# Kernel tuning notes

Hardware: AMD Instinct MI355X
Metric: run time of the kernel (lower is better)

## Reference

```python
import jax, jax.numpy as jnp
import numpy as np

# FlowNetC correlation hyperparameters (match init_kwargs)
PAD = 20          # pad_size
KSIZE = 1         # kernel_size (1x1 patches -> plain per-pixel dot over channels)
MAXD = 20         # max_displacement
STRIDE1 = 1       # output grid stride
STRIDE2 = 2       # displacement stride


def setup_inputs() -> dict:
    key = jax.random.key(0)
    k1, k2 = jax.random.split(key)
    B, C, H, W = 16, 256, 48, 64
    return {
        "input1": jax.random.normal(k1, (B, C, H, W), dtype=jnp.float32),
        "input2": jax.random.normal(k2, (B, C, H, W), dtype=jnp.float32),
    }


def _correlation(in1, in2):
    B, C, H, W = in1.shape
    # pad input2 spatially; max_displacement == pad_size so every shifted
    # window of size (H, W) stays in-bounds of the padded map.
    pad2 = jnp.pad(in2, ((0, 0), (0, 0), (PAD, PAD), (PAD, PAD)))
    disps = np.arange(-MAXD, MAXD + 1, STRIDE2)  # 21 offsets per axis
    offsets = jnp.asarray(
        [(PAD + dy, PAD + dx) for dy in disps for dx in disps], dtype=jnp.int32
    )  # [D=441, 2]

    in1s = in1[:, :, ::STRIDE1, ::STRIDE1]  # output-grid view of input1

    def one_displacement(off):
        # shifted (H, W) window of padded input2 at displacement (dy, dx)
        sl = jax.lax.dynamic_slice(pad2, (0, 0, off[0], off[1]), (B, C, H, W))
        sl = sl[:, :, ::STRIDE1, ::STRIDE1]
        # per-pixel dot product over channels
        return jnp.einsum('bchw,bchw->bhw', in1s, sl)

    # lax.map keeps memory low: one [B,C,H,W] slice live at a time
    out = jax.lax.map(one_displacement, offsets)  # [D, B, Ho, Wo]
    sumelems = KSIZE * KSIZE * C  # CUDA kernel normalizes by patch elem count
    return jnp.transpose(out, (1, 0, 2, 3)) / sumelems  # [B, D, Ho, Wo]


def reference(input1, input2):
    return _correlation(input1, input2)
```

## Files before the change

### kernel.cpp

```cpp
#include <hip/hip_runtime.h>
#include <stdint.h>

#define NB 16
#define NC 256
#define NH 48
#define NW 64
#define ND 21
#define HW (NH * NW)
#define ROW_ELEMS (NW * NC)
#define SOUT_LD (NW + 1)
#define SOUT_SZ (ND * SOUT_LD)
#define NXCD 8
#define NWG (NB * NH)

typedef __bf16 bf16x8 __attribute__((ext_vector_type(8)));
typedef float f32x4 __attribute__((ext_vector_type(4)));

__device__ __forceinline__ int xcd_wg(int orig) {
    return (orig & (NXCD - 1)) * (NWG / NXCD) + (orig >> 3);
}

__device__ __forceinline__ int sw_addr(int x, int chunk) {
    int cs = (chunk & ~7) | ((chunk ^ x) & 7);
    return x * 256 + (cs << 3);
}
__device__ __forceinline__ int posx(int x) { return ((x & 1) << 5) | (x >> 1); }

__device__ __forceinline__ int frag_off(int w, int kb, int l) {
    return w * 4096 + kb * 512 + ((l ^ ((w & 3) << 1)) << 3);
}

__device__ __forceinline__ bf16x8 load_pack8(const float* __restrict__ p, int cbase) {
    bf16x8 v;
#pragma unroll
    for (int j = 0; j < 8; ++j)
        v[j] = (__bf16)p[(size_t)(cbase + j) * HW];
    return v;
}

__global__ void __launch_bounds__(256, 4)
convert_in2(const float* __restrict__ in2, unsigned short* __restrict__ ws) {
    __shared__ unsigned short s[ROW_ELEMS];
    const int tid = threadIdx.x;
    const int wg = xcd_wg(blockIdx.x);
    const int b = wg / NH, y = wg % NH;
    const int x = tid & 63, g0 = tid >> 6;
    const int par = x & 1, m_lo = (x >> 1) & 15, nt = x >> 5;
    const int w = (nt << 1) | par;
    const float* p = in2 + ((size_t)b * NC * NH + y) * NW + x;
#pragma unroll
    for (int i = 0; i < 8; ++i) {
        const int chunk = g0 * 8 + i;
        const int kb = chunk >> 2, quad = chunk & 3;
        const int l = (quad << 4) | m_lo;
        bf16x8 v = load_pack8(p, chunk * 8);
        *(bf16x8*)&s[frag_off(w, kb, l)] = v;
    }
    __syncthreads();
    unsigned short* wr = ws + ((size_t)b * NH + y) * ROW_ELEMS;
#pragma unroll
    for (int i = 0; i < 8; ++i) {
        const int e = (i * 256 + tid) * 8;
        *(bf16x8*)(wr + e) = *(const bf16x8*)(s + e);
    }
}

__global__ void __launch_bounds__(256, 3)
corr_main(const float* __restrict__ in1, const unsigned short* __restrict__ ws,
          float* __restrict__ out) {
    __shared__ unsigned short s1[ROW_ELEMS];
    __shared__ float sout[2 * SOUT_SZ];
    const int tid  = threadIdx.x;
    const int wg   = xcd_wg(blockIdx.x);
    const int b    = wg / NH, y = wg % NH;
    const int lane = tid & 63, wave = tid >> 6;
    const int m_lo = lane & 15, quad = lane >> 4;
    const int par  = wave & 1, nt = wave >> 1;

    {
        const int x = tid & 63, g0 = tid >> 6;
        const int px = posx(x);
        const float* p = in1 + ((size_t)b * NC * NH + y) * NW + x;
#pragma unroll
        for (int i = 0; i < 8; ++i) {
            const int chunk = g0 * 8 + i;
            bf16x8 v = load_pack8(p, chunk * 8);
            *(bf16x8*)&s1[sw_addr(px, chunk)] = v;
        }
    }
    for (int i = tid; i < 2 * SOUT_SZ; i += 256) sout[i] = 0.0f;

    const int d0 = (y >= 20) ? 0 : (21 - y) >> 1;
    const int d1 = min(20, (67 - y) >> 1);
    const unsigned short* wsb = ws + (size_t)b * NH * ROW_ELEMS;
    const int slice_off = frag_off(wave, 0, lane);

    auto load_b = [&](bf16x8 (&bf)[8], int dyi) {
        const unsigned short* row = wsb + (size_t)(y - 20 + 2 * dyi) * ROW_ELEMS + slice_off;
#pragma unroll
        for (int kb = 0; kb < 8; ++kb)
            bf[kb] = *(const bf16x8*)&row[kb * 512];
    };

    bf16x8 bfA[8], bfB[8];
    load_b(bfA, d0);
    __syncthreads();

    bf16x8 afrag[2][8];
#pragma unroll
    for (int mm = 0; mm < 2; ++mm) {
        const int pos = par * 32 + 16 * mm + m_lo;
#pragma unroll
        for (int kb = 0; kb < 8; ++kb)
            afrag[mm][kb] = *(const bf16x8*)&s1[sw_addr(pos, 4 * kb + quad)];
    }

    float* outbase = out + (((size_t)b * (ND * ND)) * NH + (size_t)y) * NW;
    for (int dyi = 0; dyi < ND; ++dyi) {
        if (dyi >= d0 && dyi <= d1) continue;
        float* ob = outbase + (size_t)dyi * ND * HW;
        for (int i = tid; i < ND * NW; i += 256)
            __builtin_nontemporal_store(0.0f, &ob[(size_t)(i >> 6) * HW + (i & 63)]);
    }

    const float scale = 1.0f / 256.0f;
    const int xq  = 4 * quad;
    const int xph = 16 * nt + m_lo;
    const int dx0 = tid & 63;
    const int dp0 = tid >> 6;

    auto step = [&](bf16x8 (&bc)[8], bf16x8 (&bn)[8], int dyi, int cb) {
        if (dyi < d1) load_b(bn, dyi + 1);

        const bool have = dyi > d0;
        float dv[6];
        float* sp = sout + (cb ^ 1) * SOUT_SZ;
        if (have) {
#pragma unroll
            for (int k = 0; k < 6; ++k) {
                const int i = dx0 + (dp0 + 4 * k) * 64;
                if (i < ND * NW) dv[k] = sp[(dp0 + 4 * k) * SOUT_LD + dx0];
            }
        }

        f32x4 acc0 = {0.f, 0.f, 0.f, 0.f}, acc1 = {0.f, 0.f, 0.f, 0.f};
#pragma unroll
        for (int kb = 0; kb < 8; ++kb) {
            acc0 = __builtin_amdgcn_mfma_f32_16x16x32_bf16(afrag[0][kb], bc[kb], acc0, 0, 0, 0);
            acc1 = __builtin_amdgcn_mfma_f32_16x16x32_bf16(afrag[1][kb], bc[kb], acc1, 0, 0, 0);
        }

        if (have) {
            float* ob = outbase + (size_t)(dyi - 1) * ND * HW;
#pragma unroll
            for (int k = 0; k < 6; ++k) {
                const int i = dx0 + (dp0 + 4 * k) * 64;
                if (i < ND * NW)
                    __builtin_nontemporal_store(dv[k] * scale,
                                                &ob[(size_t)(dp0 + 4 * k) * HW + dx0]);
            }
        }

        float* sb = sout + cb * SOUT_SZ;
#pragma unroll
        for (int r = 0; r < 4; ++r) {
            {
                const int xh = xq + r;
                const int dxi = xph - xh + 10;
                if ((unsigned)dxi <= 20u) sb[dxi * SOUT_LD + 2 * xh + par] = acc0[r];
            }
            {
                const int xh = 16 + xq + r;
                const int dxi = xph - xh + 10;
                if ((unsigned)dxi <= 20u) sb[dxi * SOUT_LD + 2 * xh + par] = acc1[r];
            }
        }
        __asm__ __volatile__("s_waitcnt lgkmcnt(0)\n\ts_barrier" ::: "memory");
    };

    int dyi = d0, last;
    while (true) {
        step(bfA, bfB, dyi, 0);
        if (++dyi > d1) { last = 0; break; }
        step(bfB, bfA, dyi, 1);
        if (++dyi > d1) { last = 1; break; }
    }
    {
        float* sp = sout + last * SOUT_SZ;
        float* ob = outbase + (size_t)d1 * ND * HW;
        for (int i = tid; i < ND * NW; i += 256) {
            const int pl = i >> 6, x = i & 63;
            __builtin_nontemporal_store(sp[pl * SOUT_LD + x] * scale, &ob[(size_t)pl * HW + x]);
        }
    }
}

__global__ void __launch_bounds__(256, 2)
corr_fallback(const float* __restrict__ in1, const float* __restrict__ in2,
              float* __restrict__ out) {
    __shared__ unsigned short s1[ROW_ELEMS];
    __shared__ unsigned short s2[ROW_ELEMS];
    const int tid = threadIdx.x;
    const int b = blockIdx.x / NH, y = blockIdx.x % NH;
    const int lane = tid & 63, wave = tid >> 6;
    const int m_lo = lane & 15, quad = lane >> 4;
    const int asub = wave >> 1, bsub = wave & 1;
    {
        const int x = tid & 63, g0 = tid >> 6;
        const float* p = in1 + ((size_t)b * NC * NH + y) * NW + x;
        for (int i = 0; i < 8; ++i) {
            const int chunk = g0 * 8 + i;
            bf16x8 v = load_pack8(p, chunk * 8);
            *(bf16x8*)&s1[sw_addr(x, chunk)] = v;
        }
    }
    __syncthreads();
    bf16x8 afrag[2][8];
    for (int mm = 0; mm < 2; ++mm) {
        const int x = 32 * asub + 16 * mm + m_lo;
        for (int kb = 0; kb < 8; ++kb)
            afrag[mm][kb] = *(const bf16x8*)&s1[sw_addr(x, 4 * kb + quad)];
    }
    const float scale = 1.0f / 256.0f;
    for (int dyi = 0; dyi < ND; ++dyi) {
        const int ys = y + 2 * dyi - 20;
        float* ob = out + (((size_t)b * (ND * ND) + (size_t)dyi * ND) * NH + y) * NW;
        if ((unsigned)ys >= (unsigned)NH) {
            for (int i = tid; i < ND * NW; i += 256)
                ob[(size_t)(i >> 6) * HW + (i & 63)] = 0.0f;
            continue;
        }
        __syncthreads();
        {
            const int x = tid & 63, g0 = tid >> 6;
            const float* p = in2 + ((size_t)b * NC * NH + ys) * NW + x;
            for (int i = 0; i < 8; ++i) {
                const int chunk = g0 * 8 + i;
                bf16x8 v = load_pack8(p, chunk * 8);
                *(bf16x8*)&s2[sw_addr(x, chunk)] = v;
            }
        }
        __syncthreads();
        f32x4 acc[2][2];
        for (int mm = 0; mm < 2; ++mm)
            for (int nn = 0; nn < 2; ++nn) acc[mm][nn] = (f32x4){0.f, 0.f, 0.f, 0.f};
        for (int nn = 0; nn < 2; ++nn) {
            const int xpp = 32 * bsub + 16 * nn + m_lo;
            for (int kb = 0; kb < 8; ++kb) {
                bf16x8 bfrag = *(const bf16x8*)&s2[sw_addr(xpp, 4 * kb + quad)];
                acc[0][nn] = __builtin_amdgcn_mfma_f32_16x16x32_bf16(afrag[0][kb], bfrag, acc[0][nn], 0, 0, 0);
                acc[1][nn] = __builtin_amdgcn_mfma_f32_16x16x32_bf16(afrag[1][kb], bfrag, acc[1][nn], 0, 0, 0);
            }
        }
        for (int mm = 0; mm < 2; ++mm)
            for (int nn = 0; nn < 2; ++nn) {
                const int xb = 32 * asub + 16 * mm + 4 * quad;
                const int xpp = 32 * bsub + 16 * nn + m_lo;
                for (int r = 0; r < 4; ++r) {
                    const int x = xb + r, d = xpp - x;
                    if (d >= -20 && d <= 20 && !(d & 1))
                        ob[(size_t)((d + 20) >> 1) * HW + x] = acc[mm][nn][r] * scale;
                }
            }
        for (int i = tid; i < ND * 20; i += 256) {
            const int dxi = i / 20, j = i - dxi * 20;
            const int dx = 2 * dxi - 20, a = dx < 0 ? -dx : dx;
            if (j < a) {
                const int x = dx < 0 ? j : (NW - dx + j);
                ob[(size_t)dxi * HW + x] = 0.0f;
            }
        }
    }
}

extern "C" void kernel_launch(void* const* d_in, const int* in_sizes, int n_in,
                              void* d_out, int out_size, void* d_ws, size_t ws_size,
                              hipStream_t stream) {
    const float* in1 = (const float*)d_in[0];
    const float* in2 = (const float*)d_in[1];
    float* out = (float*)d_out;
    const size_t need = (size_t)NB * NH * ROW_ELEMS * sizeof(unsigned short);
    if (ws_size >= need) {
        convert_in2<<<dim3(NWG), dim3(256), 0, stream>>>(in2, (unsigned short*)d_ws);
        corr_main<<<dim3(NWG), dim3(256), 0, stream>>>(in1, (const unsigned short*)d_ws, out);
    } else {
        corr_fallback<<<dim3(NWG), dim3(256), 0, stream>>>(in1, in2, out);
    }
}
```

Measured before the change: 55.74 us.

## Process two vertical displacements per barrier phase in correlation kernel

Restructures the main loop so each phase computes two dy displacements at once, with three rotating B-fragment register buffers and a 4-slot shared output buffer, halving the number of barriers and store phases. A-fragments are now reloaded from LDS inside the MFMA loop instead of being held in registers, to free registers for the extra buffers. Output padding (SOUT_LD) is dropped, which may add LDS bank conflicts, and LDS use doubles, which could lower occupancy.

Result: slower. 69.61 us (+24.9%).

```diff
diff --git a/kernel.cpp b/kernel.cpp
--- a/kernel.cpp
+++ b/kernel.cpp
@@ -8,8 +8,6 @@
 #define ND 21
 #define HW (NH * NW)
 #define ROW_ELEMS (NW * NC)
-#define SOUT_LD (NW + 1)
-#define SOUT_SZ (ND * SOUT_LD)
 #define NXCD 8
 #define NWG (NB * NH)
 
@@ -69,7 +67,7 @@
 corr_main(const float* __restrict__ in1, const unsigned short* __restrict__ ws,
           float* __restrict__ out) {
     __shared__ unsigned short s1[ROW_ELEMS];
-    __shared__ float sout[2 * SOUT_SZ];
+    __shared__ float sout[4][ND * NW];
     const int tid  = threadIdx.x;
     const int wg   = xcd_wg(blockIdx.x);
     const int b    = wg / NH, y = wg % NH;
@@ -88,7 +86,7 @@
             *(bf16x8*)&s1[sw_addr(px, chunk)] = v;
         }
     }
-    for (int i = tid; i < 2 * SOUT_SZ; i += 256) sout[i] = 0.0f;
+    for (int i = tid; i < 4 * ND * NW; i += 256) ((float*)sout)[i] = 0.0f;
 
     const int d0 = (y >= 20) ? 0 : (21 - y) >> 1;
     const int d1 = min(20, (67 - y) >> 1);
@@ -102,18 +100,10 @@
             bf[kb] = *(const bf16x8*)&row[kb * 512];
     };
 
-    bf16x8 bfA[8], bfB[8];
-    load_b(bfA, d0);
+    bf16x8 B0[8], B1[8], B2[8];
+    load_b(B0, d0);
+    load_b(B1, d0 + 1);
     __syncthreads();
-
-    bf16x8 afrag[2][8];
-#pragma unroll
-    for (int mm = 0; mm < 2; ++mm) {
-        const int pos = par * 32 + 16 * mm + m_lo;
-#pragma unroll
-        for (int kb = 0; kb < 8; ++kb)
-            afrag[mm][kb] = *(const bf16x8*)&s1[sw_addr(pos, 4 * kb + quad)];
-    }
 
     float* outbase = out + (((size_t)b * (ND * ND)) * NH + (size_t)y) * NW;
     for (int dyi = 0; dyi < ND; ++dyi) {
@@ -124,73 +114,103 @@
     }
 
     const float scale = 1.0f / 256.0f;
-    const int xq  = 4 * quad;
-    const int xph = 16 * nt + m_lo;
-    const int dx0 = tid & 63;
-    const int dp0 = tid >> 6;
-
-    auto step = [&](bf16x8 (&bc)[8], bf16x8 (&bn)[8], int dyi, int cb) {
-        if (dyi < d1) load_b(bn, dyi + 1);
-
-        const bool have = dyi > d0;
-        float dv[6];
-        float* sp = sout + (cb ^ 1) * SOUT_SZ;
+    const int xq    = 4 * quad;
+    const int xph   = 16 * nt + m_lo;
+    const int apos0 = par * 32 + m_lo;
+    const int apos1 = par * 32 + 16 + m_lo;
+
+    auto phase = [&](bf16x8 (&bc0)[8], bf16x8 (&bc1)[8], bf16x8 (&bn)[8],
+                     int p, bool have, int cb) {
+        const bool two = (p + 1 <= d1);
+
+        float dva[6], dvb[6];
         if (have) {
-#pragma unroll
-            for (int k = 0; k < 6; ++k) {
-                const int i = dx0 + (dp0 + 4 * k) * 64;
-                if (i < ND * NW) dv[k] = sp[(dp0 + 4 * k) * SOUT_LD + dx0];
-            }
-        }
-
-        f32x4 acc0 = {0.f, 0.f, 0.f, 0.f}, acc1 = {0.f, 0.f, 0.f, 0.f};
+            const float* spa = sout[2 * (cb ^ 1)];
+            const float* spb = sout[2 * (cb ^ 1) + 1];
+#pragma unroll
+            for (int k = 0; k < 5; ++k) {
+                dva[k] = spa[(wave + 4 * k) * NW + lane];
+                dvb[k] = spb[(wave + 4 * k) * NW + lane];
+            }
+            if (wave == 0) { dva[5] = spa[20 * NW + lane]; dvb[5] = spb[20 * NW + lane]; }
+        }
+
+        f32x4 a00 = {0,0,0,0}, a01 = {0,0,0,0}, a10 = {0,0,0,0}, a11 = {0,0,0,0};
 #pragma unroll
         for (int kb = 0; kb < 8; ++kb) {
-            acc0 = __builtin_amdgcn_mfma_f32_16x16x32_bf16(afrag[0][kb], bc[kb], acc0, 0, 0, 0);
-            acc1 = __builtin_amdgcn_mfma_f32_16x16x32_bf16(afrag[1][kb], bc[kb], acc1, 0, 0, 0);
-        }
+            bf16x8 af0 = *(const bf16x8*)&s1[sw_addr(apos0, 4 * kb + quad)];
+            bf16x8 af1 = *(const bf16x8*)&s1[sw_addr(apos1, 4 * kb + quad)];
+            a00 = __builtin_amdgcn_mfma_f32_16x16x32_bf16(af0, bc0[kb], a00, 0, 0, 0);
+            a01 = __builtin_amdgcn_mfma_f32_16x16x32_bf16(af1, bc0[kb], a01, 0, 0, 0);
+            a10 = __builtin_amdgcn_mfma_f32_16x16x32_bf16(af0, bc1[kb], a10, 0, 0, 0);
+            a11 = __builtin_amdgcn_mfma_f32_16x16x32_bf16(af1, bc1[kb], a11, 0, 0, 0);
+        }
+
+        if (p + 2 <= d1) load_b(bn, p + 2);
+        if (p + 3 <= d1) load_b(bc1, p + 3);
 
         if (have) {
-            float* ob = outbase + (size_t)(dyi - 1) * ND * HW;
-#pragma unroll
-            for (int k = 0; k < 6; ++k) {
-                const int i = dx0 + (dp0 + 4 * k) * 64;
-                if (i < ND * NW)
-                    __builtin_nontemporal_store(dv[k] * scale,
-                                                &ob[(size_t)(dp0 + 4 * k) * HW + dx0]);
-            }
-        }
-
-        float* sb = sout + cb * SOUT_SZ;
+            float* oba = outbase + (size_t)(p - 2) * ND * HW;
+            float* obb = outbase + (size_t)(p - 1) * ND * HW;
+#pragma unroll
+            for (int k = 0; k < 5; ++k) {
+                __builtin_nontemporal_store(dva[k] * scale, &oba[(size_t)(wave + 4 * k) * HW + lane]);
+                __builtin_nontemporal_store(dvb[k] * scale, &obb[(size_t)(wave + 4 * k) * HW + lane]);
+            }
+            if (wave == 0) {
+                __builtin_nontemporal_store(dva[5] * scale, &oba[(size_t)20 * HW + lane]);
+                __builtin_nontemporal_store(dvb[5] * scale, &obb[(size_t)20 * HW + lane]);
+            }
+        }
+
+        float* sb0 = sout[2 * cb];
+        float* sb1 = sout[2 * cb + 1];
 #pragma unroll
         for (int r = 0; r < 4; ++r) {
             {
                 const int xh = xq + r;
                 const int dxi = xph - xh + 10;
-                if ((unsigned)dxi <= 20u) sb[dxi * SOUT_LD + 2 * xh + par] = acc0[r];
+                if ((unsigned)dxi <= 20u) {
+                    const int a = dxi * NW + 2 * xh + par;
+                    sb0[a] = a00[r];
+                    if (two) sb1[a] = a10[r];
+                }
             }
             {
                 const int xh = 16 + xq + r;
                 const int dxi = xph - xh + 10;
-                if ((unsigned)dxi <= 20u) sb[dxi * SOUT_LD + 2 * xh + par] = acc1[r];
+                if ((unsigned)dxi <= 20u) {
+                    const int a = dxi * NW + 2 * xh + par;
+                    sb0[a] = a01[r];
+                    if (two) sb1[a] = a11[r];
+                }
             }
         }
         __asm__ __volatile__("s_waitcnt lgkmcnt(0)\n\ts_barrier" ::: "memory");
     };
 
-    int dyi = d0, last;
+    int p = d0;
+    bool have = false;
+    int lastcb, lastp;
     while (true) {
-        step(bfA, bfB, dyi, 0);
-        if (++dyi > d1) { last = 0; break; }
-        step(bfB, bfA, dyi, 1);
-        if (++dyi > d1) { last = 1; break; }
+        phase(B0, B1, B2, p, have, 0);
+        have = true; lastp = p; p += 2;
+        if (p > d1) { lastcb = 0; break; }
+        phase(B2, B1, B0, p, true, 1);
+        lastp = p; p += 2;
+        if (p > d1) { lastcb = 1; break; }
     }
     {
-        float* sp = sout + last * SOUT_SZ;
-        float* ob = outbase + (size_t)d1 * ND * HW;
+        const bool two = (lastp + 1 <= d1);
+        const float* spa = sout[2 * lastcb];
+        const float* spb = sout[2 * lastcb + 1];
+        float* oba = outbase + (size_t)lastp * ND * HW;
+        float* obb = outbase + (size_t)(lastp + 1) * ND * HW;
         for (int i = tid; i < ND * NW; i += 256) {
             const int pl = i >> 6, x = i & 63;
-            __builtin_nontemporal_store(sp[pl * SOUT_LD + x] * scale, &ob[(size_t)pl * HW + x]);
+            __builtin_nontemporal_store(spa[pl * NW + x] * scale, &oba[(size_t)pl * HW + x]);
+            if (two)
+                __builtin_nontemporal_store(spb[pl * NW + x] * scale, &obb[(size_t)pl * HW + x]);
         }
     }
 }
```

## Split correlation workgroups by x-half and dy-half for more parallelism

Applied to the files above, without the earlier changes.

Each (batch,row) workgroup of corr_main is split into four: two halves of the x range (mt) and two halves of the dy displacement range. Each block now holds half of input1's row in LDS and runs one MFMA accumulator per step instead of two. It reuses the same shared buffer for the input fragment and the output staging, which cuts LDS use and raises the occupancy target to 4. In exchange, the B-fragment rows are loaded redundantly by the x-half blocks, and extra barriers plus four times as many launches add overhead.

Result: slower. 58.96 us (+5.8%).

```diff
diff --git a/kernel.cpp b/kernel.cpp
--- a/kernel.cpp
+++ b/kernel.cpp
@@ -8,23 +8,27 @@
 #define ND 21
 #define HW (NH * NW)
 #define ROW_ELEMS (NW * NC)
-#define SOUT_LD (NW + 1)
-#define SOUT_SZ (ND * SOUT_LD)
 #define NXCD 8
 #define NWG (NB * NH)
+#define SO_LD 33
+#define SO_SZ (ND * SO_LD)
 
 typedef __bf16 bf16x8 __attribute__((ext_vector_type(8)));
 typedef float f32x4 __attribute__((ext_vector_type(4)));
 
 __device__ __forceinline__ int xcd_wg(int orig) {
     return (orig & (NXCD - 1)) * (NWG / NXCD) + (orig >> 3);
+}
+
+__device__ __forceinline__ int swh(int lpos, int chunk) {
+    int cs = (chunk & ~7) | ((chunk ^ lpos) & 7);
+    return lpos * 256 + (cs << 3);
 }
 
 __device__ __forceinline__ int sw_addr(int x, int chunk) {
     int cs = (chunk & ~7) | ((chunk ^ x) & 7);
     return x * 256 + (cs << 3);
 }
-__device__ __forceinline__ int posx(int x) { return ((x & 1) << 5) | (x >> 1); }
 
 __device__ __forceinline__ int frag_off(int w, int kb, int l) {
     return w * 4096 + kb * 512 + ((l ^ ((w & 3) << 1)) << 3);
@@ -65,36 +69,59 @@
     }
 }
 
-__global__ void __launch_bounds__(256, 3)
+__global__ void __launch_bounds__(256, 4)
 corr_main(const float* __restrict__ in1, const unsigned short* __restrict__ ws,
           float* __restrict__ out) {
-    __shared__ unsigned short s1[ROW_ELEMS];
-    __shared__ float sout[2 * SOUT_SZ];
+    __shared__ __align__(16) unsigned char smem[16384];
+    unsigned short* s1h = (unsigned short*)smem;
+    float* soutf = (float*)smem;
+
     const int tid  = threadIdx.x;
-    const int wg   = xcd_wg(blockIdx.x);
+    const int xcd  = blockIdx.x & 7;
+    const int u    = blockIdx.x >> 3;
+    const int wg   = xcd * (NWG / NXCD) + (u >> 2);
+    const int mt   = u & 1, half = (u >> 1) & 1;
     const int b    = wg / NH, y = wg % NH;
     const int lane = tid & 63, wave = tid >> 6;
     const int m_lo = lane & 15, quad = lane >> 4;
     const int par  = wave & 1, nt = wave >> 1;
 
-    {
-        const int x = tid & 63, g0 = tid >> 6;
-        const int px = posx(x);
-        const float* p = in1 + ((size_t)b * NC * NH + y) * NW + x;
-#pragma unroll
-        for (int i = 0; i < 8; ++i) {
-            const int chunk = g0 * 8 + i;
-            bf16x8 v = load_pack8(p, chunk * 8);
-            *(bf16x8*)&s1[sw_addr(px, chunk)] = v;
-        }
-    }
-    for (int i = tid; i < 2 * SOUT_SZ; i += 256) sout[i] = 0.0f;
-
     const int d0 = (y >= 20) ? 0 : (21 - y) >> 1;
     const int d1 = min(20, (67 - y) >> 1);
+    const int r0 = half * 11, r1 = half ? ND : 11;
+    const int e0 = max(d0, r0), e1 = min(d1, r1 - 1);
+
+    float* outbase = out + (((size_t)b * (ND * ND)) * NH + (size_t)y) * NW;
+    const int xl = tid & 31, dpz = tid >> 5;
+
+    auto zero_plane = [&](int dyi) {
+        float* ob = outbase + (size_t)dyi * ND * HW;
+#pragma unroll
+        for (int k = 0; k < 3; ++k) {
+            const int dxi = dpz + 8 * k;
+            if (dxi < ND)
+                __builtin_nontemporal_store(0.0f, &ob[(size_t)dxi * HW + 32 * mt + xl]);
+        }
+    };
+    if (e0 > e1) {
+        for (int dyi = r0; dyi < r1; ++dyi) zero_plane(dyi);
+        return;
+    }
+
+    {
+        const int x = 32 * mt + (tid & 31), g0 = tid >> 5;
+        const int lpos = ((x & 1) << 4) | ((x >> 1) & 15);
+        const float* p = in1 + ((size_t)b * NC * NH + y) * NW + x;
+#pragma unroll
+        for (int i = 0; i < 4; ++i) {
+            const int chunk = g0 * 4 + i;
+            bf16x8 v = load_pack8(p, chunk * 8);
+            *(bf16x8*)&s1h[swh(lpos, chunk)] = v;
+        }
+    }
+
     const unsigned short* wsb = ws + (size_t)b * NH * ROW_ELEMS;
     const int slice_off = frag_off(wave, 0, lane);
-
     auto load_b = [&](bf16x8 (&bf)[8], int dyi) {
         const unsigned short* row = wsb + (size_t)(y - 20 + 2 * dyi) * ROW_ELEMS + slice_off;
 #pragma unroll
@@ -102,95 +129,90 @@
             bf[kb] = *(const bf16x8*)&row[kb * 512];
     };
 
-    bf16x8 bfA[8], bfB[8];
-    load_b(bfA, d0);
-    __syncthreads();
-
-    bf16x8 afrag[2][8];
-#pragma unroll
-    for (int mm = 0; mm < 2; ++mm) {
-        const int pos = par * 32 + 16 * mm + m_lo;
+    bf16x8 B0[8], B1[8];
+    load_b(B0, e0);
+    load_b(B1, min(e0 + 1, e1));
+
+    for (int dyi = r0; dyi < r1; ++dyi)
+        if (dyi < e0 || dyi > e1) zero_plane(dyi);
+
+    __asm__ __volatile__("s_waitcnt lgkmcnt(0)\n\ts_barrier" ::: "memory");
+
+    bf16x8 afrag[8];
+    {
+        const int lpa = par * 16 + m_lo;
 #pragma unroll
         for (int kb = 0; kb < 8; ++kb)
-            afrag[mm][kb] = *(const bf16x8*)&s1[sw_addr(pos, 4 * kb + quad)];
-    }
-
-    float* outbase = out + (((size_t)b * (ND * ND)) * NH + (size_t)y) * NW;
-    for (int dyi = 0; dyi < ND; ++dyi) {
-        if (dyi >= d0 && dyi <= d1) continue;
-        float* ob = outbase + (size_t)dyi * ND * HW;
-        for (int i = tid; i < ND * NW; i += 256)
-            __builtin_nontemporal_store(0.0f, &ob[(size_t)(i >> 6) * HW + (i & 63)]);
-    }
+            afrag[kb] = *(const bf16x8*)&s1h[swh(lpa, 4 * kb + quad)];
+    }
+    __asm__ __volatile__("s_waitcnt lgkmcnt(0)\n\ts_barrier" ::: "memory");
+
+    for (int i = tid; i < 2 * SO_SZ; i += 256) soutf[i] = 0.0f;
+    __asm__ __volatile__("s_waitcnt lgkmcnt(0)\n\ts_barrier" ::: "memory");
 
     const float scale = 1.0f / 256.0f;
     const int xq  = 4 * quad;
     const int xph = 16 * nt + m_lo;
-    const int dx0 = tid & 63;
-    const int dp0 = tid >> 6;
-
-    auto step = [&](bf16x8 (&bc)[8], bf16x8 (&bn)[8], int dyi, int cb) {
-        if (dyi < d1) load_b(bn, dyi + 1);
-
-        const bool have = dyi > d0;
-        float dv[6];
-        float* sp = sout + (cb ^ 1) * SOUT_SZ;
+
+    auto step = [&](bf16x8 (&bc)[8], int t, int cb, bool have) {
+        float dv[3];
+        const float* sp = soutf + (cb ^ 1) * SO_SZ;
         if (have) {
 #pragma unroll
-            for (int k = 0; k < 6; ++k) {
-                const int i = dx0 + (dp0 + 4 * k) * 64;
-                if (i < ND * NW) dv[k] = sp[(dp0 + 4 * k) * SOUT_LD + dx0];
-            }
-        }
-
-        f32x4 acc0 = {0.f, 0.f, 0.f, 0.f}, acc1 = {0.f, 0.f, 0.f, 0.f};
-#pragma unroll
-        for (int kb = 0; kb < 8; ++kb) {
-            acc0 = __builtin_amdgcn_mfma_f32_16x16x32_bf16(afrag[0][kb], bc[kb], acc0, 0, 0, 0);
-            acc1 = __builtin_amdgcn_mfma_f32_16x16x32_bf16(afrag[1][kb], bc[kb], acc1, 0, 0, 0);
-        }
+            for (int k = 0; k < 3; ++k) {
+                const int dxi = dpz + 8 * k;
+                if (dxi < ND) dv[k] = sp[dxi * SO_LD + xl];
+            }
+        }
+
+        f32x4 acc = {0.f, 0.f, 0.f, 0.f};
+#pragma unroll
+        for (int kb = 0; kb < 8; ++kb)
+            acc = __builtin_amdgcn_mfma_f32_16x16x32_bf16(afrag[kb], bc[kb], acc, 0, 0, 0);
+
+        if (t + 2 <= e1) load_b(bc, t + 2);
 
         if (have) {
-            float* ob = outbase + (size_t)(dyi - 1) * ND * HW;
-#pragma unroll
-            for (int k = 0; k < 6; ++k) {
-                const int i = dx0 + (dp0 + 4 * k) * 64;
-                if (i < ND * NW)
+            float* ob = outbase + (size_t)(t - 1) * ND * HW;
+#pragma unroll
+            for (int k = 0; k < 3; ++k) {
+                const int dxi = dpz + 8 * k;
+                if (dxi < ND)
                     __builtin_nontemporal_store(dv[k] * scale,
-                                                &ob[(size_t)(dp0 + 4 * k) * HW + dx0]);
-            }
-        }
-
-        float* sb = sout + cb * SOUT_SZ;
+                                                &ob[(size_t)dxi * HW + 32 * mt + xl]);
+            }
+        }
+
+        float* sb = soutf + cb * SO_SZ;
 #pragma unroll
         for (int r = 0; r < 4; ++r) {
-            {
-                const int xh = xq + r;
-                const int dxi = xph - xh + 10;
-                if ((unsigned)dxi <= 20u) sb[dxi * SOUT_LD + 2 * xh + par] = acc0[r];
-            }
-            {
-                const int xh = 16 + xq + r;
-                const int dxi = xph - xh + 10;
-                if ((unsigned)dxi <= 20u) sb[dxi * SOUT_LD + 2 * xh + par] = acc1[r];
-            }
+            const int lxh = xq + r;
+            const int dxi = xph - (16 * mt + lxh) + 10;
+            if ((unsigned)dxi <= 20u)
+                sb[dxi * SO_LD + 2 * lxh + par] = acc[r];
         }
         __asm__ __volatile__("s_waitcnt lgkmcnt(0)\n\ts_barrier" ::: "memory");
     };
 
-    int dyi = d0, last;
-    while (true) {
-        step(bfA, bfB, dyi, 0);
-        if (++dyi > d1) { last = 0; break; }
-        step(bfB, bfA, dyi, 1);
-        if (++dyi > d1) { last = 1; break; }
+    int t = e0, cb = 0, lastcb = 0;
+    bool have = false;
+    for (;;) {
+        step(B0, t, cb, have); lastcb = cb;
+        if (++t > e1) break;
+        cb ^= 1; have = true;
+        step(B1, t, cb, have); lastcb = cb;
+        if (++t > e1) break;
+        cb ^= 1;
     }
     {
-        float* sp = sout + last * SOUT_SZ;
-        float* ob = outbase + (size_t)d1 * ND * HW;
-        for (int i = tid; i < ND * NW; i += 256) {
-            const int pl = i >> 6, x = i & 63;
-            __builtin_nontemporal_store(sp[pl * SOUT_LD + x] * scale, &ob[(size_t)pl * HW + x]);
+        const float* sp = soutf + lastcb * SO_SZ;
+        float* ob = outbase + (size_t)e1 * ND * HW;
+#pragma unroll
+        for (int k = 0; k < 3; ++k) {
+            const int dxi = dpz + 8 * k;
+            if (dxi < ND)
+                __builtin_nontemporal_store(sp[dxi * SO_LD + xl] * scale,
+                                            &ob[(size_t)dxi * HW + 32 * mt + xl]);
         }
     }
 }
@@ -282,7 +304,7 @@
     const size_t need = (size_t)NB * NH * ROW_ELEMS * sizeof(unsigned short);
     if (ws_size >= need) {
         convert_in2<<<dim3(NWG), dim3(256), 0, stream>>>(in2, (unsigned short*)d_ws);
-        corr_main<<<dim3(NWG), dim3(256), 0, stream>>>(in1, (const unsigned short*)d_ws, out);
+        corr_main<<<dim3(NWG * 4), dim3(256), 0, stream>>>(in1, (const unsigned short*)d_ws, out);
     } else {
         corr_fallback<<<dim3(NWG), dim3(256), 0, stream>>>(in1, in2, out);
     }
```

## Share each input2 row across six output rows per workgroup via LDS

Applied to the files above, without the earlier changes.

The correlation kernel is restructured so each 768-thread workgroup handles three pairs of same-parity output rows (six rows) of one batch, split into two halves over the displacement range. Each input2 row is loaded once into LDS and reused by all six rows' MFMA tiles, instead of every row-workgroup re-reading its own 21 rows from global memory. This cuts redundant global/L2 traffic for the B operand. The cost is fewer, larger workgroups (256), more barriers per step, a 64 KB LDS footprint that limits occupancy, and idle waves whenever a shared row falls outside a given output row's displacement window.

Result: faster. 49.38 us (-11.4%).

```diff
diff --git a/kernel.cpp b/kernel.cpp
--- a/kernel.cpp
+++ b/kernel.cpp
@@ -8,10 +8,10 @@
 #define ND 21
 #define HW (NH * NW)
 #define ROW_ELEMS (NW * NC)
-#define SOUT_LD (NW + 1)
-#define SOUT_SZ (ND * SOUT_LD)
 #define NXCD 8
 #define NWG (NB * NH)
+#define SO_LD 65
+#define SO_SZ (ND * SO_LD)
 
 typedef __bf16 bf16x8 __attribute__((ext_vector_type(8)));
 typedef float f32x4 __attribute__((ext_vector_type(4)));
@@ -65,133 +65,156 @@
     }
 }
 
-__global__ void __launch_bounds__(256, 3)
+__global__ void __launch_bounds__(768, 3)
 corr_main(const float* __restrict__ in1, const unsigned short* __restrict__ ws,
           float* __restrict__ out) {
-    __shared__ unsigned short s1[ROW_ELEMS];
-    __shared__ float sout[2 * SOUT_SZ];
+    __shared__ __align__(16) unsigned char smem[65536];
+    unsigned short* bbuf  = (unsigned short*)smem;
+    float*          soutf = (float*)(smem + 32768);
+    unsigned short* areg0 = (unsigned short*)smem;
+    unsigned short* areg1 = (unsigned short*)(smem + 32768);
+
     const int tid  = threadIdx.x;
-    const int wg   = xcd_wg(blockIdx.x);
-    const int b    = wg / NH, y = wg % NH;
+    const int bid  = blockIdx.x;
+    const int xcd  = bid & 7;
+    const int u    = bid >> 3;
+    const int b    = 2 * xcd + (u >> 4);
+    const int v    = u & 15;
+    const int P    = v & 1, g = (v >> 1) & 3, half = v >> 3;
+    const int y0   = 12 * g + P;
     const int lane = tid & 63, wave = tid >> 6;
     const int m_lo = lane & 15, quad = lane >> 4;
-    const int par  = wave & 1, nt = wave >> 1;
-
+    const int par  = wave & 1, yy = wave >> 1;
+    const int y    = y0 + 2 * yy;
+
+    const int lo = max(y0 - 20, P);
+    const int hi = min(y0 + 30, 46 + P);
+    const int n  = ((hi - lo) >> 1) + 1;
+    const int n0 = (n + 1) >> 1;
+    const int lo_h = half ? (lo + 2 * n0) : lo;
+    const int nh   = half ? (n - n0) : n0;
+
+    const unsigned short* wsb = ws + (size_t)b * NH * ROW_ELEMS;
+
+    bf16x8 Bst[3];
     {
-        const int x = tid & 63, g0 = tid >> 6;
-        const int px = posx(x);
-        const float* p = in1 + ((size_t)b * NC * NH + y) * NW + x;
-#pragma unroll
-        for (int i = 0; i < 8; ++i) {
-            const int chunk = g0 * 8 + i;
-            bf16x8 v = load_pack8(p, chunk * 8);
-            *(bf16x8*)&s1[sw_addr(px, chunk)] = v;
-        }
-    }
-    for (int i = tid; i < 2 * SOUT_SZ; i += 256) sout[i] = 0.0f;
-
-    const int d0 = (y >= 20) ? 0 : (21 - y) >> 1;
+        const unsigned short* row = wsb + (size_t)lo_h * ROW_ELEMS;
+        Bst[0] = *(const bf16x8*)&row[tid * 8];
+        Bst[1] = *(const bf16x8*)&row[(768 + tid) * 8];
+        if (tid < 512) Bst[2] = *(const bf16x8*)&row[(1536 + tid) * 8];
+    }
+
+    bf16x8 afrag[2][8];
+#pragma unroll 1
+    for (int rnd = 0; rnd < 3; ++rnd) {
+        const int yA = y0 + 4 * rnd;
+#pragma unroll
+        for (int i = 0; i < 6; ++i) {
+            const int uu = i * 768 + tid;
+            if (uu < 4096) {
+                const int row = uu >> 11, cu = uu & 2047;
+                const int x = cu & 63, chunk = cu >> 6;
+                const float* p = in1 + ((size_t)b * NC * NH + (yA + 2 * row)) * NW + x;
+                bf16x8 vv = load_pack8(p, chunk * 8);
+                unsigned short* dst = row ? areg1 : areg0;
+                *(bf16x8*)&dst[sw_addr(posx(x), chunk)] = vv;
+            }
+        }
+        __asm__ __volatile__("s_waitcnt lgkmcnt(0)\n\ts_barrier" ::: "memory");
+        if ((yy >> 1) == rnd) {
+            const unsigned short* src = (yy & 1) ? areg1 : areg0;
+            const int pos0 = par * 32 + m_lo;
+#pragma unroll
+            for (int kb = 0; kb < 8; ++kb) {
+                afrag[0][kb] = *(const bf16x8*)&src[sw_addr(pos0,      4 * kb + quad)];
+                afrag[1][kb] = *(const bf16x8*)&src[sw_addr(pos0 + 16, 4 * kb + quad)];
+            }
+        }
+        __asm__ __volatile__("s_waitcnt lgkmcnt(0)\n\ts_barrier" ::: "memory");
+    }
+
+    *(bf16x8*)&bbuf[tid * 8] = Bst[0];
+    *(bf16x8*)&bbuf[(768 + tid) * 8] = Bst[1];
+    if (tid < 512) *(bf16x8*)&bbuf[(1536 + tid) * 8] = Bst[2];
+    for (int i = tid; i < 6 * SO_SZ; i += 768) soutf[i] = 0.0f;
+
+    float* outyy = out + (size_t)b * (ND * ND) * HW + (size_t)y * NW;
+    const int d0 = (y >= 20) ? 0 : ((21 - y) >> 1);
     const int d1 = min(20, (67 - y) >> 1);
-    const unsigned short* wsb = ws + (size_t)b * NH * ROW_ELEMS;
-    const int slice_off = frag_off(wave, 0, lane);
-
-    auto load_b = [&](bf16x8 (&bf)[8], int dyi) {
-        const unsigned short* row = wsb + (size_t)(y - 20 + 2 * dyi) * ROW_ELEMS + slice_off;
-#pragma unroll
-        for (int kb = 0; kb < 8; ++kb)
-            bf[kb] = *(const bf16x8*)&row[kb * 512];
-    };
-
-    bf16x8 bfA[8], bfB[8];
-    load_b(bfA, d0);
-    __syncthreads();
-
-    bf16x8 afrag[2][8];
-#pragma unroll
-    for (int mm = 0; mm < 2; ++mm) {
-        const int pos = par * 32 + 16 * mm + m_lo;
-#pragma unroll
-        for (int kb = 0; kb < 8; ++kb)
-            afrag[mm][kb] = *(const bf16x8*)&s1[sw_addr(pos, 4 * kb + quad)];
-    }
-
-    float* outbase = out + (((size_t)b * (ND * ND)) * NH + (size_t)y) * NW;
-    for (int dyi = 0; dyi < ND; ++dyi) {
-        if (dyi >= d0 && dyi <= d1) continue;
-        float* ob = outbase + (size_t)dyi * ND * HW;
-        for (int i = tid; i < ND * NW; i += 256)
-            __builtin_nontemporal_store(0.0f, &ob[(size_t)(i >> 6) * HW + (i & 63)]);
-    }
+    const int zlo = half ? (d1 + 1) : 0;
+    const int zhi = half ? ND : d0;
+    const int t2  = par * 64 + lane;
+    for (int z = zlo; z < zhi; ++z) {
+        float* ob = outyy + (size_t)z * ND * HW;
+#pragma unroll
+        for (int i = 0; i < 11; ++i) {
+            const int e = i * 128 + t2;
+            if (e < ND * NW)
+                __builtin_nontemporal_store(0.0f, &ob[(size_t)(e >> 6) * HW + (e & 63)]);
+        }
+    }
+    __asm__ __volatile__("s_waitcnt lgkmcnt(0)\n\ts_barrier" ::: "memory");
 
     const float scale = 1.0f / 256.0f;
-    const int xq  = 4 * quad;
-    const int xph = 16 * nt + m_lo;
-    const int dx0 = tid & 63;
-    const int dp0 = tid >> 6;
-
-    auto step = [&](bf16x8 (&bc)[8], bf16x8 (&bn)[8], int dyi, int cb) {
-        if (dyi < d1) load_b(bn, dyi + 1);
-
-        const bool have = dyi > d0;
-        float dv[6];
-        float* sp = sout + (cb ^ 1) * SOUT_SZ;
-        if (have) {
-#pragma unroll
-            for (int k = 0; k < 6; ++k) {
-                const int i = dx0 + (dp0 + 4 * k) * 64;
-                if (i < ND * NW) dv[k] = sp[(dp0 + 4 * k) * SOUT_LD + dx0];
-            }
-        }
-
-        f32x4 acc0 = {0.f, 0.f, 0.f, 0.f}, acc1 = {0.f, 0.f, 0.f, 0.f};
-#pragma unroll
-        for (int kb = 0; kb < 8; ++kb) {
-            acc0 = __builtin_amdgcn_mfma_f32_16x16x32_bf16(afrag[0][kb], bc[kb], acc0, 0, 0, 0);
-            acc1 = __builtin_amdgcn_mfma_f32_16x16x32_bf16(afrag[1][kb], bc[kb], acc1, 0, 0, 0);
-        }
-
-        if (have) {
-            float* ob = outbase + (size_t)(dyi - 1) * ND * HW;
-#pragma unroll
-            for (int k = 0; k < 6; ++k) {
-                const int i = dx0 + (dp0 + 4 * k) * 64;
-                if (i < ND * NW)
-                    __builtin_nontemporal_store(dv[k] * scale,
-                                                &ob[(size_t)(dp0 + 4 * k) * HW + dx0]);
-            }
-        }
-
-        float* sb = sout + cb * SOUT_SZ;
-#pragma unroll
-        for (int r = 0; r < 4; ++r) {
-            {
-                const int xh = xq + r;
-                const int dxi = xph - xh + 10;
-                if ((unsigned)dxi <= 20u) sb[dxi * SOUT_LD + 2 * xh + par] = acc0[r];
-            }
-            {
-                const int xh = 16 + xq + r;
-                const int dxi = xph - xh + 10;
-                if ((unsigned)dxi <= 20u) sb[dxi * SOUT_LD + 2 * xh + par] = acc1[r];
+    const int boff0 = frag_off((0 << 1) | par, 0, lane);
+    const int boff1 = frag_off((1 << 1) | par, 0, lane);
+
+    for (int k = 0; k < nh; ++k) {
+        const int ys = lo_h + 2 * k;
+        if (k + 1 < nh) {
+            const unsigned short* row = wsb + (size_t)(ys + 2) * ROW_ELEMS;
+            Bst[0] = *(const bf16x8*)&row[tid * 8];
+            Bst[1] = *(const bf16x8*)&row[(768 + tid) * 8];
+            if (tid < 512) Bst[2] = *(const bf16x8*)&row[(1536 + tid) * 8];
+        }
+        const int dyi = ((ys - y) >> 1) + 10;
+        const bool valid = (unsigned)dyi <= 20u;
+
+        if (valid) {
+            f32x4 a00 = {0,0,0,0}, a01 = {0,0,0,0}, a10 = {0,0,0,0}, a11 = {0,0,0,0};
+#pragma unroll
+            for (int kb = 0; kb < 8; ++kb) {
+                bf16x8 b0 = *(const bf16x8*)&bbuf[boff0 + kb * 512];
+                bf16x8 b1 = *(const bf16x8*)&bbuf[boff1 + kb * 512];
+                a00 = __builtin_amdgcn_mfma_f32_16x16x32_bf16(afrag[0][kb], b0, a00, 0, 0, 0);
+                a10 = __builtin_amdgcn_mfma_f32_16x16x32_bf16(afrag[1][kb], b0, a10, 0, 0, 0);
+                a01 = __builtin_amdgcn_mfma_f32_16x16x32_bf16(afrag[0][kb], b1, a01, 0, 0, 0);
+                a11 = __builtin_amdgcn_mfma_f32_16x16x32_bf16(afrag[1][kb], b1, a11, 0, 0, 0);
+            }
+            float* sp = soutf + yy * SO_SZ;
+#pragma unroll
+            for (int mm = 0; mm < 2; ++mm)
+#pragma unroll
+            for (int nn = 0; nn < 2; ++nn)
+#pragma unroll
+            for (int r = 0; r < 4; ++r) {
+                const int xh  = 16 * mm + 4 * quad + r;
+                const int dxi = (16 * nn + m_lo) - xh + 10;
+                const float vv = mm == 0 ? (nn == 0 ? a00[r] : a01[r])
+                                         : (nn == 0 ? a10[r] : a11[r]);
+                if ((unsigned)dxi <= 20u)
+                    sp[dxi * SO_LD + 2 * xh + par] = vv;
             }
         }
         __asm__ __volatile__("s_waitcnt lgkmcnt(0)\n\ts_barrier" ::: "memory");
-    };
-
-    int dyi = d0, last;
-    while (true) {
-        step(bfA, bfB, dyi, 0);
-        if (++dyi > d1) { last = 0; break; }
-        step(bfB, bfA, dyi, 1);
-        if (++dyi > d1) { last = 1; break; }
-    }
-    {
-        float* sp = sout + last * SOUT_SZ;
-        float* ob = outbase + (size_t)d1 * ND * HW;
-        for (int i = tid; i < ND * NW; i += 256) {
-            const int pl = i >> 6, x = i & 63;
-            __builtin_nontemporal_store(sp[pl * SOUT_LD + x] * scale, &ob[(size_t)pl * HW + x]);
-        }
+
+        if (k + 1 < nh) {
+            *(bf16x8*)&bbuf[tid * 8] = Bst[0];
+            *(bf16x8*)&bbuf[(768 + tid) * 8] = Bst[1];
+            if (tid < 512) *(bf16x8*)&bbuf[(1536 + tid) * 8] = Bst[2];
+        }
+        if (valid) {
+            const float* sp = soutf + yy * SO_SZ;
+            float* ob = outyy + (size_t)dyi * ND * HW;
+#pragma unroll
+            for (int i = 0; i < 11; ++i) {
+                const int e = i * 128 + t2;
+                if (e < ND * NW)
+                    __builtin_nontemporal_store(sp[(e >> 6) * SO_LD + (e & 63)] * scale,
+                                                &ob[(size_t)(e >> 6) * HW + (e & 63)]);
+            }
+        }
+        __asm__ __volatile__("s_waitcnt lgkmcnt(0)\n\ts_barrier" ::: "memory");
     }
 }
 
@@ -282,7 +305,7 @@
     const size_t need = (size_t)NB * NH * ROW_ELEMS * sizeof(unsigned short);
     if (ws_size >= need) {
         convert_in2<<<dim3(NWG), dim3(256), 0, stream>>>(in2, (unsigned short*)d_ws);
-        corr_main<<<dim3(NWG), dim3(256), 0, stream>>>(in1, (const unsigned short*)d_ws, out);
+        corr_main<<<dim3(256), dim3(768), 0, stream>>>(in1, (const unsigned short*)d_ws, out);
     } else {
         corr_fallback<<<dim3(NWG), dim3(256), 0, stream>>>(in1, in2, out);
     }
```
